# Kernel tuning notes

Hardware: AMD Instinct MI355X
Metric: run time of the kernel (lower is better)

The kernel has to match this reference:

```python
import jax, jax.numpy as jnp
import numpy as np

D_MODEL = 1024
NHEAD = 16
D_K = D_MODEL // NHEAD
D_FF = 4096
EPS = 1e-5


def _layer_norm(x, g, b):
    mu = jnp.mean(x, axis=-1, keepdims=True)
    var = jnp.mean(jnp.square(x - mu), axis=-1, keepdims=True)
    return (x - mu) * jax.lax.rsqrt(var + EPS) * g + b


def setup_inputs() -> dict:
    key = jax.random.key(0)
    ks = jax.random.split(key, 14)
    s = 0.02
    d = {
        'src': jax.random.normal(ks[0], (4, 2048, D_MODEL), dtype=jnp.float32),
        'Wq': jax.random.normal(ks[1], (D_MODEL, D_MODEL), dtype=jnp.float32) * s,
        'bq': jnp.zeros((D_MODEL,), jnp.float32),
        'Wk': jax.random.normal(ks[2], (D_MODEL, D_MODEL), dtype=jnp.float32) * s,
        'bk': jnp.zeros((D_MODEL,), jnp.float32),
        'Wv': jax.random.normal(ks[3], (D_MODEL, D_MODEL), dtype=jnp.float32) * s,
        'bv': jnp.zeros((D_MODEL,), jnp.float32),
        'Wo': jax.random.normal(ks[4], (D_MODEL, D_MODEL), dtype=jnp.float32) * s,
        'bo': jnp.zeros((D_MODEL,), jnp.float32),
        'W1': jax.random.normal(ks[5], (D_MODEL, D_FF), dtype=jnp.float32) * s,
        'b1': jnp.zeros((D_FF,), jnp.float32),
        'W2': jax.random.normal(ks[6], (D_FF, D_MODEL), dtype=jnp.float32) * s,
        'b2': jnp.zeros((D_MODEL,), jnp.float32),
        'ln1_g': jnp.ones((D_MODEL,), jnp.float32),
        'ln1_b': jnp.zeros((D_MODEL,), jnp.float32),
        'ln2_g': jnp.ones((D_MODEL,), jnp.float32),
        'ln2_b': jnp.zeros((D_MODEL,), jnp.float32),
    }
    return d


def reference(src, Wq, bq, Wk, bk, Wv, bv, Wo, bo, W1, b1, W2, b2,
              ln1_g, ln1_b, ln2_g, ln2_b):
    B, L, _ = src.shape
    # QKV projections -> [B, H, L, d_k]
    def heads(x, W, b):
        y = x @ W + b
        return y.reshape(B, L, NHEAD, D_K).transpose(0, 2, 1, 3)
    Q = heads(src, Wq, bq)
    K = heads(src, Wk, bk)
    V = heads(src, Wv, bv)
    # scores [B, H, Lq, Lk]
    scores = jnp.einsum('bhqd,bhkd->bhqk', Q, K) / jnp.sqrt(jnp.float32(D_K))
    attn = jax.nn.softmax(scores, axis=-1)
    ctx = jnp.einsum('bhqk,bhkd->bhqd', attn, V)
    ctx = ctx.transpose(0, 2, 1, 3).reshape(B, L, D_MODEL)
    attn_out = ctx @ Wo + bo
    x = _layer_norm(src + attn_out, ln1_g, ln1_b)
    ff = jax.nn.relu(x @ W1 + b1) @ W2 + b2
    return _layer_norm(x + ff, ln2_g, ln2_b)
```

## Files before the change

### kernel.cpp

```cpp
#include <hip/hip_runtime.h>
#include <hip/hip_bf16.h>


#define D_MODEL 1024
#define SEQ     2048
#define BATCH   4
#define NHEAD   16
#define D_FF    4096
#define M_ROWS  (BATCH * SEQ)

typedef __attribute__((ext_vector_type(8))) short bf16x8;
typedef __attribute__((ext_vector_type(4))) float f32x4;

__device__ __forceinline__ ushort f2bf(float x) {
    unsigned u = __float_as_uint(x);
    unsigned r = (u + 0x7FFFu + ((u >> 16) & 1u)) >> 16;
    return (ushort)r;
}

__device__ __forceinline__ int swz_off(int r, int q) {
    return ((r >> 1) << 6) | (((((r & 1) << 2) | q) ^ ((r >> 1) & 7)) << 3);
}

__global__ __launch_bounds__(256) void cast_kernel(
    const float* __restrict__ x, ushort* __restrict__ y)
{
    const size_t i = ((size_t)blockIdx.x * 256 + threadIdx.x) * 4;
    float4 v = *(const float4*)&x[i];
    ushort4 o;
    o.x = f2bf(v.x); o.y = f2bf(v.y); o.z = f2bf(v.z); o.w = f2bf(v.w);
    *(ushort4*)&y[i] = o;
}

__global__ __launch_bounds__(256) void transpose_cast_kernel(
    const float* __restrict__ W, ushort* __restrict__ Wt, int R, int C)
{
    __shared__ float tile[64][68];
    const int c0 = blockIdx.x * 64, r0 = blockIdx.y * 64;
    const int t  = threadIdx.x;
    const int tc  = (t & 15) * 4;
    const int tr4 = (t >> 4) * 4;
#pragma unroll
    for (int i = 0; i < 4; ++i) {
        float4 v = *(const float4*)&W[(size_t)(r0 + tr4 + i) * C + c0 + tc];
        *(float4*)&tile[tr4 + i][tc] = v;
    }
    __syncthreads();
#pragma unroll
    for (int i = 0; i < 4; ++i) {
        const int nn = tr4 + i;
        ushort4 o;
        o.x = f2bf(tile[tc + 0][nn]);
        o.y = f2bf(tile[tc + 1][nn]);
        o.z = f2bf(tile[tc + 2][nn]);
        o.w = f2bf(tile[tc + 3][nn]);
        *(ushort4*)&Wt[(size_t)(c0 + nn) * R + r0 + tc] = o;
    }
}

template <int MODE>
__global__ __launch_bounds__(256) void gemm_mfma(
    const ushort* __restrict__ A, const ushort* __restrict__ Bt,
    const float* __restrict__ bias, void* __restrict__ C,
    int M, int N, int K, float scale, int nxshift)
{
    __shared__ __attribute__((aligned(16))) ushort As[128 * 32];
    __shared__ __attribute__((aligned(16))) ushort Bs[128 * 32];

    const int t    = threadIdx.x;
    const int lane = t & 63;
    const int wave = t >> 6;

    const int bid   = blockIdx.y * gridDim.x + blockIdx.x;
    const int idx   = bid >> 3;
    const int bxs   = idx & ((1 << nxshift) - 1);
    const int bys   = (bid & 7) * (gridDim.y >> 3) + (idx >> nxshift);
    const int bm    = bys * 128;
    const int bn    = bxs * 128;

    const int wm   = (wave & 1) * 64;
    const int wn   = (wave >> 1) * 64;
    const int fr   = lane & 15;
    const int quad = lane >> 4;

    f32x4 acc[4][4];
#pragma unroll
    for (int i = 0; i < 4; ++i)
#pragma unroll
        for (int j = 0; j < 4; ++j)
            acc[i][j] = (f32x4){0.f, 0.f, 0.f, 0.f};

    for (int k0 = 0; k0 < K; k0 += 32) {
#pragma unroll
        for (int r = 0; r < 2; ++r) {
            const int s   = r * 256 + t;
            const int c   = (s & ~7) | ((s & 7) ^ ((s >> 3) & 7));
            const int row = c >> 2;
            const int kc  = (c & 3) * 8;
            __builtin_amdgcn_global_load_lds(
                (const __attribute__((address_space(1))) void*)(A + (size_t)(bm + row) * K + k0 + kc),
                (__attribute__((address_space(3))) void*)(As + s * 8), 16, 0, 0);
            __builtin_amdgcn_global_load_lds(
                (const __attribute__((address_space(1))) void*)(Bt + (size_t)(bn + row) * K + k0 + kc),
                (__attribute__((address_space(3))) void*)(Bs + s * 8), 16, 0, 0);
        }
        __syncthreads();

        bf16x8 af[4], bfr[4];
#pragma unroll
        for (int i = 0; i < 4; ++i)
            af[i] = *(const bf16x8*)&As[swz_off(wm + i * 16 + fr, quad)];
#pragma unroll
        for (int j = 0; j < 4; ++j)
            bfr[j] = *(const bf16x8*)&Bs[swz_off(wn + j * 16 + fr, quad)];

#pragma unroll
        for (int i = 0; i < 4; ++i)
#pragma unroll
            for (int j = 0; j < 4; ++j)
                acc[i][j] = __builtin_amdgcn_mfma_f32_16x16x32_bf16(af[i], bfr[j], acc[i][j], 0, 0, 0);
        __syncthreads();
    }

    const int rbase = quad * 4;
    float bcol[4];
#pragma unroll
    for (int j = 0; j < 4; ++j) bcol[j] = bias[bn + wn + j * 16 + fr];

#pragma unroll
    for (int i = 0; i < 4; ++i) {
#pragma unroll
        for (int j = 0; j < 4; ++j) {
            const int col  = bn + wn + j * 16 + fr;
            const int row0 = bm + wm + i * 16 + rbase;
            float v[4];
#pragma unroll
            for (int r = 0; r < 4; ++r) v[r] = acc[i][j][r] + bcol[j];

            if (MODE == 0) {
#pragma unroll
                for (int r = 0; r < 4; ++r)
                    ((float*)C)[(size_t)(row0 + r) * N + col] = v[r];
            } else if (MODE == 2) {
#pragma unroll
                for (int r = 0; r < 4; ++r)
                    ((ushort*)C)[(size_t)(row0 + r) * N + col] = f2bf(fmaxf(v[r], 0.f));
            } else if (MODE == 1) {
                const int h = col >> 6, d = col & 63;
#pragma unroll
                for (int r = 0; r < 4; ++r) {
                    const int row = row0 + r;
                    const int b = row >> 11, l = row & 2047;
                    ((ushort*)C)[(((size_t)(b * NHEAD + h) * SEQ + l) << 6) + d] = f2bf(v[r] * scale);
                }
            } else {
                const int b = row0 >> 11, l0 = row0 & 2047;
                const int h = col >> 6,  d = col & 63;
                ushort4 o;
                o.x = f2bf(v[0]); o.y = f2bf(v[1]); o.z = f2bf(v[2]); o.w = f2bf(v[3]);
                *(ushort4*)&((ushort*)C)[(((size_t)(b * NHEAD + h) * 64 + d) << 11) + l0] = o;
            }
        }
    }
}

__global__ __launch_bounds__(256, 3) void attn_mfma(
    const ushort* __restrict__ Q, const ushort* __restrict__ K,
    const ushort* __restrict__ Vt, ushort* __restrict__ CTX)
{
    __shared__ __attribute__((aligned(16))) ushort Ks[64 * 64];
    __shared__ __attribute__((aligned(16))) ushort Vs[64 * 64];
    __shared__ __attribute__((aligned(16))) ushort Ps[128 * 64];

    const int t    = threadIdx.x;
    const int lane = t & 63;
    const int w    = t >> 6;
    const int l15  = lane & 15;
    const int quad = lane >> 4;

    const int bid = blockIdx.y * gridDim.x + blockIdx.x;
    const int idx = bid >> 3;
    const int bh  = (bid & 7) * 8 + (idx >> 4);
    const int q0  = (idx & 15) * 128;

    bf16x8 afq[2][2];
    const ushort* Qbase = Q + ((size_t)bh * SEQ + q0 + w * 32) * 64;
#pragma unroll
    for (int i = 0; i < 2; ++i)
#pragma unroll
        for (int ks = 0; ks < 2; ++ks)
            afq[i][ks] = *(const bf16x8*)&Qbase[(i * 16 + l15) * 64 + quad * 8 + ks * 32];

    f32x4 oacc[2][4];
#pragma unroll
    for (int i = 0; i < 2; ++i)
#pragma unroll
        for (int d = 0; d < 4; ++d) oacc[i][d] = (f32x4){0.f, 0.f, 0.f, 0.f};
    float lrun[2][4];
#pragma unroll
    for (int i = 0; i < 2; ++i)
#pragma unroll
        for (int r = 0; r < 4; ++r) lrun[i][r] = 0.f;

    const ushort* Kb  = K  + ((size_t)bh * SEQ) * 64;
    const ushort* Vtb = Vt + ((size_t)bh * 64) * SEQ;

    const int srow0 = t >> 3;
    const int sc8   = t & 7;

    for (int kk0 = 0; kk0 < SEQ; kk0 += 64) {
        bf16x8 kv0 = *(const bf16x8*)&Kb[(size_t)(kk0 + srow0) * 64 + sc8 * 8];
        bf16x8 kv1 = *(const bf16x8*)&Kb[(size_t)(kk0 + srow0 + 32) * 64 + sc8 * 8];
        bf16x8 vv0 = *(const bf16x8*)&Vtb[(size_t)srow0 * SEQ + kk0 + sc8 * 8];
        bf16x8 vv1 = *(const bf16x8*)&Vtb[(size_t)(srow0 + 32) * SEQ + kk0 + sc8 * 8];

        __syncthreads();

        {
            const int pr0 = (srow0 & 3) * 16 + (srow0 >> 2);
            const int pr1 = ((srow0 + 32) & 3) * 16 + ((srow0 + 32) >> 2);
            *(bf16x8*)&Ks[pr0 * 64 + ((sc8 ^ (pr0 & 7)) << 3)] = kv0;
            *(bf16x8*)&Ks[pr1 * 64 + ((sc8 ^ (pr1 & 7)) << 3)] = kv1;
            *(bf16x8*)&Vs[srow0 * 64 + ((sc8 ^ (srow0 & 7)) << 3)] = vv0;
            *(bf16x8*)&Vs[(srow0 + 32) * 64 + ((sc8 ^ ((srow0 + 32) & 7)) << 3)] = vv1;
        }
        __syncthreads();

        f32x4 sacc[2][4];
#pragma unroll
        for (int i = 0; i < 2; ++i)
#pragma unroll
            for (int j = 0; j < 4; ++j) sacc[i][j] = (f32x4){0.f, 0.f, 0.f, 0.f};
        const int swz0 = (quad ^ (l15 & 7)) << 3;
        const int swz1 = ((quad + 4) ^ (l15 & 7)) << 3;
#pragma unroll
        for (int j = 0; j < 4; ++j) {
            const int krow = (j * 16 + l15) * 64;
            bf16x8 bk0 = *(const bf16x8*)&Ks[krow + swz0];
            bf16x8 bk1 = *(const bf16x8*)&Ks[krow + swz1];
            sacc[0][j] = __builtin_amdgcn_mfma_f32_16x16x32_bf16(afq[0][0], bk0, sacc[0][j], 0, 0, 0);
            sacc[0][j] = __builtin_amdgcn_mfma_f32_16x16x32_bf16(afq[0][1], bk1, sacc[0][j], 0, 0, 0);
            sacc[1][j] = __builtin_amdgcn_mfma_f32_16x16x32_bf16(afq[1][0], bk0, sacc[1][j], 0, 0, 0);
            sacc[1][j] = __builtin_amdgcn_mfma_f32_16x16x32_bf16(afq[1][1], bk1, sacc[1][j], 0, 0, 0);
        }

#pragma unroll
        for (int i = 0; i < 2; ++i) {
#pragma unroll
            for (int r = 0; r < 4; ++r) {
                const float p0 = __expf(sacc[i][0][r]);
                const float p1 = __expf(sacc[i][1][r]);
                const float p2 = __expf(sacc[i][2][r]);
                const float p3 = __expf(sacc[i][3][r]);
                lrun[i][r] += (p0 + p1) + (p2 + p3);
                const unsigned u0 = __builtin_amdgcn_perm(
                    __float_as_uint(p1), __float_as_uint(p0), 0x07060302u);
                const unsigned u1 = __builtin_amdgcn_perm(
                    __float_as_uint(p3), __float_as_uint(p2), 0x07060302u);
                const int prow = w * 32 + i * 16 + quad * 4 + r;
                const int off = prow * 64 + (((l15 >> 1) ^ (prow & 7)) << 3) + (l15 & 1) * 4;
                *(unsigned long long*)&Ps[off] =
                    (unsigned long long)u0 | ((unsigned long long)u1 << 32);
            }
        }

        bf16x8 ap[2][2];
#pragma unroll
        for (int i = 0; i < 2; ++i) {
            const int prow = (w * 32 + i * 16 + l15) * 64;
            ap[i][0] = *(const bf16x8*)&Ps[prow + swz0];
            ap[i][1] = *(const bf16x8*)&Ps[prow + swz1];
        }
#pragma unroll
        for (int dt = 0; dt < 4; ++dt) {
            const int vrow = (dt * 16 + l15) * 64;
            bf16x8 bv0 = *(const bf16x8*)&Vs[vrow + swz0];
            bf16x8 bv1 = *(const bf16x8*)&Vs[vrow + swz1];
            oacc[0][dt] = __builtin_amdgcn_mfma_f32_16x16x32_bf16(ap[0][0], bv0, oacc[0][dt], 0, 0, 0);
            oacc[0][dt] = __builtin_amdgcn_mfma_f32_16x16x32_bf16(ap[0][1], bv1, oacc[0][dt], 0, 0, 0);
            oacc[1][dt] = __builtin_amdgcn_mfma_f32_16x16x32_bf16(ap[1][0], bv0, oacc[1][dt], 0, 0, 0);
            oacc[1][dt] = __builtin_amdgcn_mfma_f32_16x16x32_bf16(ap[1][1], bv1, oacc[1][dt], 0, 0, 0);
        }
    }

    const int b = bh >> 4, h = bh & 15;
#pragma unroll
    for (int i = 0; i < 2; ++i) {
#pragma unroll
        for (int r = 0; r < 4; ++r) {
            float l = lrun[i][r];
#pragma unroll
            for (int m = 1; m < 16; m <<= 1) l += __shfl_xor(l, m, 64);
            const float inv = 1.f / l;
            const int tok = q0 + w * 32 + i * 16 + quad * 4 + r;
            ushort* op = CTX + ((size_t)(b * SEQ + tok)) * D_MODEL + h * 64;
#pragma unroll
            for (int dt = 0; dt < 4; ++dt)
                op[dt * 16 + l15] = f2bf(oacc[i][dt][r] * inv);
        }
    }
}

template <bool WRITE_BF>
__global__ __launch_bounds__(256) void ln_kernel(
    const float* __restrict__ y, const float* __restrict__ res,
    const float* __restrict__ g, const float* __restrict__ bta,
    float* __restrict__ out, ushort* __restrict__ out_bf)
{
    __shared__ float red[4];
    const int t = threadIdx.x;
    const size_t base = (size_t)blockIdx.x * D_MODEL + t * 4;

    float4 a = *(const float4*)&y[base];
    float4 r = *(const float4*)&res[base];
    const float v0 = a.x + r.x, v1 = a.y + r.y, v2 = a.z + r.z, v3 = a.w + r.w;

    float s = v0 + v1 + v2 + v3;
#pragma unroll
    for (int o = 32; o > 0; o >>= 1) s += __shfl_down(s, o, 64);
    if ((t & 63) == 0) red[t >> 6] = s;
    __syncthreads();
    const float mu = (red[0] + red[1] + red[2] + red[3]) * (1.f / 1024.f);

    const float d0 = v0 - mu, d1 = v1 - mu, d2 = v2 - mu, d3 = v3 - mu;
    float sq = d0 * d0 + d1 * d1 + d2 * d2 + d3 * d3;
#pragma unroll
    for (int o = 32; o > 0; o >>= 1) sq += __shfl_down(sq, o, 64);
    __syncthreads();
    if ((t & 63) == 0) red[t >> 6] = sq;
    __syncthreads();
    const float var  = (red[0] + red[1] + red[2] + red[3]) * (1.f / 1024.f);
    const float rstd = rsqrtf(var + 1e-5f);

    const int c = t * 4;
    float4 gv = *(const float4*)&g[c];
    float4 bv = *(const float4*)&bta[c];
    float4 o4;
    o4.x = d0 * rstd * gv.x + bv.x;
    o4.y = d1 * rstd * gv.y + bv.y;
    o4.z = d2 * rstd * gv.z + bv.z;
    o4.w = d3 * rstd * gv.w + bv.w;
    *(float4*)&out[base] = o4;
    if (WRITE_BF) {
        ushort4 ob;
        ob.x = f2bf(o4.x); ob.y = f2bf(o4.y); ob.z = f2bf(o4.z); ob.w = f2bf(o4.w);
        *(ushort4*)&out_bf[base] = ob;
    }
}

extern "C" void kernel_launch(void* const* d_in, const int* in_sizes, int n_in,
                              void* d_out, int out_size, void* d_ws, size_t ws_size,
                              hipStream_t stream)
{
    const float* src = (const float*)d_in[0];
    const float* Wq  = (const float*)d_in[1];  const float* bq = (const float*)d_in[2];
    const float* Wk  = (const float*)d_in[3];  const float* bk = (const float*)d_in[4];
    const float* Wv  = (const float*)d_in[5];  const float* bv = (const float*)d_in[6];
    const float* Wo  = (const float*)d_in[7];  const float* bo = (const float*)d_in[8];
    const float* W1  = (const float*)d_in[9];  const float* b1 = (const float*)d_in[10];
    const float* W2  = (const float*)d_in[11]; const float* b2 = (const float*)d_in[12];
    const float* g1  = (const float*)d_in[13]; const float* be1 = (const float*)d_in[14];
    const float* g2  = (const float*)d_in[15]; const float* be2 = (const float*)d_in[16];
    float* out = (float*)d_out;

    char* ws = (char*)d_ws;
    const size_t MB = 1024 * 1024;
    ushort* Qb   = (ushort*)(ws);
    ushort* Kb   = (ushort*)(ws + 16 * MB);
    ushort* Vtb  = (ushort*)(ws + 32 * MB);
    ushort* CTXb = (ushort*)(ws + 48 * MB);
    ushort* FFb  = (ushort*)(ws);
    float*  Xf   = (float*) (ws + 64 * MB);
    ushort* X1b  = (ushort*)(ws + 96 * MB);
    ushort* SRCb = (ushort*)(ws + 112 * MB);
    ushort* W1t  = (ushort*)(ws + 112 * MB);
    ushort* W2t  = (ushort*)(ws + 120 * MB);
    ushort* Wqt  = (ushort*)(ws + 128 * MB);
    ushort* Wkt  = (ushort*)(ws + 130 * MB);
    ushort* Wvt  = (ushort*)(ws + 132 * MB);
    ushort* Wot  = (ushort*)(ws + 134 * MB);

    dim3 blk(256);

    cast_kernel<<<dim3(M_ROWS * D_MODEL / 1024), blk, 0, stream>>>(src, SRCb);
    transpose_cast_kernel<<<dim3(16, 16), blk, 0, stream>>>(Wq, Wqt, D_MODEL, D_MODEL);
    transpose_cast_kernel<<<dim3(16, 16), blk, 0, stream>>>(Wk, Wkt, D_MODEL, D_MODEL);
    transpose_cast_kernel<<<dim3(16, 16), blk, 0, stream>>>(Wv, Wvt, D_MODEL, D_MODEL);
    transpose_cast_kernel<<<dim3(16, 16), blk, 0, stream>>>(Wo, Wot, D_MODEL, D_MODEL);

    gemm_mfma<1><<<dim3(8, 64), blk, 0, stream>>>(SRCb, Wqt, bq, Qb, M_ROWS, D_MODEL, D_MODEL, 0.125f, 3);
    gemm_mfma<1><<<dim3(8, 64), blk, 0, stream>>>(SRCb, Wkt, bk, Kb, M_ROWS, D_MODEL, D_MODEL, 1.0f, 3);
    gemm_mfma<3><<<dim3(8, 64), blk, 0, stream>>>(SRCb, Wvt, bv, Vtb, M_ROWS, D_MODEL, D_MODEL, 1.0f, 3);

    transpose_cast_kernel<<<dim3(64, 16), blk, 0, stream>>>(W1, W1t, D_MODEL, D_FF);
    transpose_cast_kernel<<<dim3(16, 64), blk, 0, stream>>>(W2, W2t, D_FF, D_MODEL);

    attn_mfma<<<dim3(SEQ / 128, BATCH * NHEAD), blk, 0, stream>>>(Qb, Kb, Vtb, CTXb);

    gemm_mfma<0><<<dim3(8, 64), blk, 0, stream>>>(CTXb, Wot, bo, Xf, M_ROWS, D_MODEL, D_MODEL, 1.0f, 3);

    ln_kernel<true><<<M_ROWS, blk, 0, stream>>>(Xf, src, g1, be1, Xf, X1b);

    gemm_mfma<2><<<dim3(32, 64), blk, 0, stream>>>(X1b, W1t, b1, FFb, M_ROWS, D_FF, D_MODEL, 1.0f, 5);

    gemm_mfma<0><<<dim3(8, 64), blk, 0, stream>>>(FFb, W2t, b2, out, M_ROWS, D_MODEL, D_FF, 1.0f, 3);

    ln_kernel<false><<<M_ROWS, blk, 0, stream>>>(out, Xf, g2, be2, out, nullptr);
}
```

Measured before the change: 570.8 us.

## Fuse QKV projections into one GEMM, batch weight casts, use 64-row tiles for N=1024 GEMMs

Merges the four per-weight transpose-cast launches into one 3D-grid kernel and concatenates Wq/Wk/Wv into a single transposed weight, so the Q, K and V projections run as one GEMM with N=3072. The epilogue picks bias, scale and output layout per column third. The GEMM gains a TM template so the Wo and W2 GEMMs (N=1024) use 64-row tiles, doubling their block count for better CU occupancy, at the cost of less A/B reuse per block. Workgroup swizzling now uses general nx division instead of a shift.

```diff
diff --git a/kernel.cpp b/kernel.cpp
--- a/kernel.cpp
+++ b/kernel.cpp
@@ -58,41 +58,75 @@
     }
 }
 
-template <int MODE>
+__global__ __launch_bounds__(256) void transpose_cast4_kernel(
+    const float* __restrict__ Wq, const float* __restrict__ Wk,
+    const float* __restrict__ Wv, const float* __restrict__ Wo,
+    ushort* __restrict__ Wqkvt, ushort* __restrict__ Wot)
+{
+    const int z = blockIdx.z;
+    const float* W = (z == 0) ? Wq : (z == 1) ? Wk : (z == 2) ? Wv : Wo;
+    ushort* out = (z < 3) ? (Wqkvt + (size_t)z * 1024 * 1024) : Wot;
+
+    __shared__ float tile[64][68];
+    const int c0 = blockIdx.x * 64, r0 = blockIdx.y * 64;
+    const int t  = threadIdx.x;
+    const int tc  = (t & 15) * 4;
+    const int tr4 = (t >> 4) * 4;
+#pragma unroll
+    for (int i = 0; i < 4; ++i) {
+        float4 v = *(const float4*)&W[(size_t)(r0 + tr4 + i) * 1024 + c0 + tc];
+        *(float4*)&tile[tr4 + i][tc] = v;
+    }
+    __syncthreads();
+#pragma unroll
+    for (int i = 0; i < 4; ++i) {
+        const int nn = tr4 + i;
+        ushort4 o;
+        o.x = f2bf(tile[tc + 0][nn]);
+        o.y = f2bf(tile[tc + 1][nn]);
+        o.z = f2bf(tile[tc + 2][nn]);
+        o.w = f2bf(tile[tc + 3][nn]);
+        *(ushort4*)&out[(size_t)(c0 + nn) * 1024 + r0 + tc] = o;
+    }
+}
+
+template <int MODE, int TM>
 __global__ __launch_bounds__(256) void gemm_mfma(
     const ushort* __restrict__ A, const ushort* __restrict__ Bt,
-    const float* __restrict__ bias, void* __restrict__ C,
-    int M, int N, int K, float scale, int nxshift)
-{
-    __shared__ __attribute__((aligned(16))) ushort As[128 * 32];
+    const float* __restrict__ bias0, const float* __restrict__ bias1,
+    const float* __restrict__ bias2, void* __restrict__ C,
+    int M, int N, int K, int nx)
+{
+    __shared__ __attribute__((aligned(16))) ushort As[TM * 32];
     __shared__ __attribute__((aligned(16))) ushort Bs[128 * 32];
 
     const int t    = threadIdx.x;
     const int lane = t & 63;
     const int wave = t >> 6;
 
-    const int bid   = blockIdx.y * gridDim.x + blockIdx.x;
-    const int idx   = bid >> 3;
-    const int bxs   = idx & ((1 << nxshift) - 1);
-    const int bys   = (bid & 7) * (gridDim.y >> 3) + (idx >> nxshift);
-    const int bm    = bys * 128;
-    const int bn    = bxs * 128;
-
-    const int wm   = (wave & 1) * 64;
+    const int bid = blockIdx.y * gridDim.x + blockIdx.x;
+    const int idx = bid >> 3;
+    const int bxs = idx % nx;
+    const int bys = (bid & 7) * (gridDim.y >> 3) + idx / nx;
+    const int bm  = bys * TM;
+    const int bn  = bxs * 128;
+
+    constexpr int WI = TM / 32;
+    const int wm   = (wave & 1) * (TM / 2);
     const int wn   = (wave >> 1) * 64;
     const int fr   = lane & 15;
     const int quad = lane >> 4;
 
-    f32x4 acc[4][4];
-#pragma unroll
-    for (int i = 0; i < 4; ++i)
+    f32x4 acc[WI][4];
+#pragma unroll
+    for (int i = 0; i < WI; ++i)
 #pragma unroll
         for (int j = 0; j < 4; ++j)
             acc[i][j] = (f32x4){0.f, 0.f, 0.f, 0.f};
 
     for (int k0 = 0; k0 < K; k0 += 32) {
 #pragma unroll
-        for (int r = 0; r < 2; ++r) {
+        for (int r = 0; r < TM / 64; ++r) {
             const int s   = r * 256 + t;
             const int c   = (s & ~7) | ((s & 7) ^ ((s >> 3) & 7));
             const int row = c >> 2;
@@ -100,22 +134,29 @@
             __builtin_amdgcn_global_load_lds(
                 (const __attribute__((address_space(1))) void*)(A + (size_t)(bm + row) * K + k0 + kc),
                 (__attribute__((address_space(3))) void*)(As + s * 8), 16, 0, 0);
+        }
+#pragma unroll
+        for (int r = 0; r < 2; ++r) {
+            const int s   = r * 256 + t;
+            const int c   = (s & ~7) | ((s & 7) ^ ((s >> 3) & 7));
+            const int row = c >> 2;
+            const int kc  = (c & 3) * 8;
             __builtin_amdgcn_global_load_lds(
                 (const __attribute__((address_space(1))) void*)(Bt + (size_t)(bn + row) * K + k0 + kc),
                 (__attribute__((address_space(3))) void*)(Bs + s * 8), 16, 0, 0);
         }
         __syncthreads();
 
-        bf16x8 af[4], bfr[4];
-#pragma unroll
-        for (int i = 0; i < 4; ++i)
+        bf16x8 af[WI], bfr[4];
+#pragma unroll
+        for (int i = 0; i < WI; ++i)
             af[i] = *(const bf16x8*)&As[swz_off(wm + i * 16 + fr, quad)];
 #pragma unroll
         for (int j = 0; j < 4; ++j)
             bfr[j] = *(const bf16x8*)&Bs[swz_off(wn + j * 16 + fr, quad)];
 
 #pragma unroll
-        for (int i = 0; i < 4; ++i)
+        for (int i = 0; i < WI; ++i)
 #pragma unroll
             for (int j = 0; j < 4; ++j)
                 acc[i][j] = __builtin_amdgcn_mfma_f32_16x16x32_bf16(af[i], bfr[j], acc[i][j], 0, 0, 0);
@@ -123,19 +164,25 @@
     }
 
     const int rbase = quad * 4;
-    float bcol[4];
-#pragma unroll
-    for (int j = 0; j < 4; ++j) bcol[j] = bias[bn + wn + j * 16 + fr];
-
-#pragma unroll
-    for (int i = 0; i < 4; ++i) {
-#pragma unroll
-        for (int j = 0; j < 4; ++j) {
-            const int col  = bn + wn + j * 16 + fr;
+#pragma unroll
+    for (int j = 0; j < 4; ++j) {
+        const int col   = bn + wn + j * 16 + fr;
+        const int third = (bn + wn + j * 16) >> 10;
+        float bc;
+        float sc = 1.f;
+        if (MODE == 4) {
+            const float* bp = (third == 0) ? bias0 : (third == 1) ? bias1 : bias2;
+            bc = bp[col & 1023];
+            if (third == 0) sc = 0.125f;
+        } else {
+            bc = bias0[col];
+        }
+#pragma unroll
+        for (int i = 0; i < WI; ++i) {
             const int row0 = bm + wm + i * 16 + rbase;
             float v[4];
 #pragma unroll
-            for (int r = 0; r < 4; ++r) v[r] = acc[i][j][r] + bcol[j];
+            for (int r = 0; r < 4; ++r) v[r] = (acc[i][j][r] + bc) * sc;
 
             if (MODE == 0) {
 #pragma unroll
@@ -145,20 +192,24 @@
 #pragma unroll
                 for (int r = 0; r < 4; ++r)
                     ((ushort*)C)[(size_t)(row0 + r) * N + col] = f2bf(fmaxf(v[r], 0.f));
-            } else if (MODE == 1) {
-                const int h = col >> 6, d = col & 63;
-#pragma unroll
-                for (int r = 0; r < 4; ++r) {
-                    const int row = row0 + r;
-                    const int b = row >> 11, l = row & 2047;
-                    ((ushort*)C)[(((size_t)(b * NHEAD + h) * SEQ + l) << 6) + d] = f2bf(v[r] * scale);
+            } else {
+                const int lc = col & 1023;
+                const int h  = lc >> 6, d = lc & 63;
+                if (third < 2) {
+                    ushort* base = (ushort*)C + (size_t)third * 8 * 1024 * 1024;
+#pragma unroll
+                    for (int r = 0; r < 4; ++r) {
+                        const int row = row0 + r;
+                        const int b = row >> 11, l = row & 2047;
+                        base[(((size_t)(b * NHEAD + h) * SEQ + l) << 6) + d] = f2bf(v[r]);
+                    }
+                } else {
+                    ushort* base = (ushort*)C + (size_t)16 * 1024 * 1024;
+                    const int b = row0 >> 11, l0 = row0 & 2047;
+                    ushort4 o;
+                    o.x = f2bf(v[0]); o.y = f2bf(v[1]); o.z = f2bf(v[2]); o.w = f2bf(v[3]);
+                    *(ushort4*)&base[(((size_t)(b * NHEAD + h) * 64 + d) << 11) + l0] = o;
                 }
-            } else {
-                const int b = row0 >> 11, l0 = row0 & 2047;
-                const int h = col >> 6,  d = col & 63;
-                ushort4 o;
-                o.x = f2bf(v[0]); o.y = f2bf(v[1]); o.z = f2bf(v[2]); o.w = f2bf(v[3]);
-                *(ushort4*)&((ushort*)C)[(((size_t)(b * NHEAD + h) * 64 + d) << 11) + l0] = o;
             }
         }
     }
@@ -365,45 +416,42 @@
 
     char* ws = (char*)d_ws;
     const size_t MB = 1024 * 1024;
-    ushort* Qb   = (ushort*)(ws);
-    ushort* Kb   = (ushort*)(ws + 16 * MB);
-    ushort* Vtb  = (ushort*)(ws + 32 * MB);
-    ushort* CTXb = (ushort*)(ws + 48 * MB);
-    ushort* FFb  = (ushort*)(ws);
-    float*  Xf   = (float*) (ws + 64 * MB);
-    ushort* X1b  = (ushort*)(ws + 96 * MB);
-    ushort* SRCb = (ushort*)(ws + 112 * MB);
-    ushort* W1t  = (ushort*)(ws + 112 * MB);
-    ushort* W2t  = (ushort*)(ws + 120 * MB);
-    ushort* Wqt  = (ushort*)(ws + 128 * MB);
-    ushort* Wkt  = (ushort*)(ws + 130 * MB);
-    ushort* Wvt  = (ushort*)(ws + 132 * MB);
-    ushort* Wot  = (ushort*)(ws + 134 * MB);
+    ushort* Qb    = (ushort*)(ws);
+    ushort* Kb    = (ushort*)(ws + 16 * MB);
+    ushort* Vtb   = (ushort*)(ws + 32 * MB);
+    ushort* CTXb  = (ushort*)(ws + 48 * MB);
+    ushort* FFb   = (ushort*)(ws);
+    float*  Xf    = (float*) (ws + 64 * MB);
+    ushort* X1b   = (ushort*)(ws + 96 * MB);
+    ushort* SRCb  = (ushort*)(ws + 112 * MB);
+    ushort* W1t   = (ushort*)(ws + 112 * MB);
+    ushort* W2t   = (ushort*)(ws + 120 * MB);
+    ushort* Wqkvt = (ushort*)(ws + 128 * MB);
+    ushort* Wot   = (ushort*)(ws + 134 * MB);
 
     dim3 blk(256);
 
     cast_kernel<<<dim3(M_ROWS * D_MODEL / 1024), blk, 0, stream>>>(src, SRCb);
-    transpose_cast_kernel<<<dim3(16, 16), blk, 0, stream>>>(Wq, Wqt, D_MODEL, D_MODEL);
-    transpose_cast_kernel<<<dim3(16, 16), blk, 0, stream>>>(Wk, Wkt, D_MODEL, D_MODEL);
-    transpose_cast_kernel<<<dim3(16, 16), blk, 0, stream>>>(Wv, Wvt, D_MODEL, D_MODEL);
-    transpose_cast_kernel<<<dim3(16, 16), blk, 0, stream>>>(Wo, Wot, D_MODEL, D_MODEL);
-
-    gemm_mfma<1><<<dim3(8, 64), blk, 0, stream>>>(SRCb, Wqt, bq, Qb, M_ROWS, D_MODEL, D_MODEL, 0.125f, 3);
-    gemm_mfma<1><<<dim3(8, 64), blk, 0, stream>>>(SRCb, Wkt, bk, Kb, M_ROWS, D_MODEL, D_MODEL, 1.0f, 3);
-    gemm_mfma<3><<<dim3(8, 64), blk, 0, stream>>>(SRCb, Wvt, bv, Vtb, M_ROWS, D_MODEL, D_MODEL, 1.0f, 3);
+    transpose_cast4_kernel<<<dim3(16, 16, 4), blk, 0, stream>>>(Wq, Wk, Wv, Wo, Wqkvt, Wot);
+
+    gemm_mfma<4, 128><<<dim3(24, 64), blk, 0, stream>>>(
+        SRCb, Wqkvt, bq, bk, bv, Qb, M_ROWS, 3 * D_MODEL, D_MODEL, 24);
 
     transpose_cast_kernel<<<dim3(64, 16), blk, 0, stream>>>(W1, W1t, D_MODEL, D_FF);
     transpose_cast_kernel<<<dim3(16, 64), blk, 0, stream>>>(W2, W2t, D_FF, D_MODEL);
 
     attn_mfma<<<dim3(SEQ / 128, BATCH * NHEAD), blk, 0, stream>>>(Qb, Kb, Vtb, CTXb);
 
-    gemm_mfma<0><<<dim3(8, 64), blk, 0, stream>>>(CTXb, Wot, bo, Xf, M_ROWS, D_MODEL, D_MODEL, 1.0f, 3);
+    gemm_mfma<0, 64><<<dim3(8, 128), blk, 0, stream>>>(
+        CTXb, Wot, bo, nullptr, nullptr, Xf, M_ROWS, D_MODEL, D_MODEL, 8);
 
     ln_kernel<true><<<M_ROWS, blk, 0, stream>>>(Xf, src, g1, be1, Xf, X1b);
 
-    gemm_mfma<2><<<dim3(32, 64), blk, 0, stream>>>(X1b, W1t, b1, FFb, M_ROWS, D_FF, D_MODEL, 1.0f, 5);
-
-    gemm_mfma<0><<<dim3(8, 64), blk, 0, stream>>>(FFb, W2t, b2, out, M_ROWS, D_MODEL, D_FF, 1.0f, 3);
+    gemm_mfma<2, 128><<<dim3(32, 64), blk, 0, stream>>>(
+        X1b, W1t, b1, nullptr, nullptr, FFb, M_ROWS, D_FF, D_MODEL, 32);
+
+    gemm_mfma<0, 64><<<dim3(8, 128), blk, 0, stream>>>(
+        FFb, W2t, b2, nullptr, nullptr, out, M_ROWS, D_MODEL, D_FF, 8);
 
     ln_kernel<false><<<M_ROWS, blk, 0, stream>>>(out, Xf, g2, be2, out, nullptr);
 }
```

Result: faster. 553.5 us (-3.0%).
